# Optimization experiments

Hardware: AMD Instinct MI355X
Metric: run time of the kernel (lower is better)

The kernel has to match this reference:

```python
import jax, jax.numpy as jnp
import numpy as np
import math

B, L, D, K = 4, 2048, 1024, 3
PAD = K // 2
EPS_LN = 1e-5
EPS_NORM = 1e-12


def dwsep_conv(x_bld, dw, dwb, pw, pwb):
    # x_bld: [B, L, D] -> depthwise conv over L (groups=D) then pointwise 1x1
    x = jnp.transpose(x_bld, (0, 2, 1))  # [B, D, L]
    y = jax.lax.conv_general_dilated(
        x, dw, window_strides=(1,), padding=[(PAD, PAD)],
        feature_group_count=D, dimension_numbers=("NCH", "OIH", "NCH"))
    y = y + dwb[None, :, None]
    y = jnp.einsum("bcl,oc->bol", y, pw) + pwb[None, :, None]
    return jnp.transpose(y, (0, 2, 1))  # [B, L, D]


def l2norm(x):
    n = jnp.sqrt(jnp.sum(x * x, axis=-1, keepdims=True))
    return x / jnp.maximum(n, EPS_NORM)


def layernorm(x, g, b):
    mu = jnp.mean(x, axis=-1, keepdims=True)
    var = jnp.mean((x - mu) ** 2, axis=-1, keepdims=True)
    return (x - mu) * jax.lax.rsqrt(var + EPS_LN) * g + b


def setup_inputs() -> dict:
    key = jax.random.key(0)
    ks = jax.random.split(key, 24)
    s = 0.02
    def w(k, shape, scale=s):
        return (jax.random.normal(k, shape, dtype=jnp.float32) * scale)
    inp = {
        "x": jax.random.normal(ks[0], (B, L, D), dtype=jnp.float32),
        "wq": w(ks[1], (D, D)), "bq": jnp.zeros((D,), jnp.float32),
        "wk": w(ks[2], (D, D)), "bk": jnp.zeros((D,), jnp.float32),
        "wv": w(ks[3], (D, D)), "bv": jnp.zeros((D,), jnp.float32),
        "dwq": w(ks[4], (D, 1, K), 0.1), "dwq_b": jnp.zeros((D,), jnp.float32),
        "pwq": w(ks[5], (D, D)), "pwq_b": jnp.zeros((D,), jnp.float32),
        "dwk": w(ks[6], (D, 1, K), 0.1), "dwk_b": jnp.zeros((D,), jnp.float32),
        "pwk": w(ks[7], (D, D)), "pwk_b": jnp.zeros((D,), jnp.float32),
        "dwv": w(ks[8], (D, 1, K), 0.1), "dwv_b": jnp.zeros((D,), jnp.float32),
        "pwv": w(ks[9], (D, D)), "pwv_b": jnp.zeros((D,), jnp.float32),
        "wg": w(ks[10], (D, D)), "bg": jnp.zeros((D,), jnp.float32),
        "wo": w(ks[11], (D, D)), "bo": jnp.zeros((D,), jnp.float32),
        "mem_w": w(ks[12], (D, D)),
        "ln_g": jnp.ones((D,), jnp.float32),
        "ln_b": jnp.zeros((D,), jnp.float32),
    }
    return inp


def reference(x, wq, bq, wk, bk, wv, bv,
              dwq, dwq_b, pwq, pwq_b,
              dwk, dwk_b, pwk, pwk_b,
              dwv, dwv_b, pwv, pwv_b,
              wg, bg, wo, bo, mem_w, ln_g, ln_b):
    residual = x
    Q = jax.nn.silu(jnp.einsum("bld,ed->ble", x, wq) + bq)
    Kt = jax.nn.silu(jnp.einsum("bld,ed->ble", x, wk) + bk)
    V = jax.nn.silu(jnp.einsum("bld,ed->ble", x, wv) + bv)
    Q = dwsep_conv(Q, dwq, dwq_b, pwq, pwq_b)
    Kt = dwsep_conv(Kt, dwk, dwk_b, pwk, pwk_b)
    V = dwsep_conv(V, dwv, dwv_b, pwv, pwv_b)
    Qn = l2norm(Q)
    Kn = l2norm(Kt)
    scores = jnp.einsum("bqd,bkd->bqk", Qn, Kn) / math.sqrt(D)
    attn = jax.nn.softmax(scores, axis=-1)
    attn_out = jnp.einsum("bqk,bkd->bqd", attn, V)
    gate = jax.nn.sigmoid(jnp.einsum("bld,ed->ble", attn_out, wg) + bg)
    gated = gate * attn_out
    out = jnp.einsum("bld,ed->ble", gated, wo) + bo + residual
    out = layernorm(out, ln_g, ln_b)
    mem_pred = jnp.einsum("bld,de->ble", Kn, mem_w)
    mem_loss = jnp.mean((mem_pred - V) ** 2)
    return (out, mem_loss)
```

## Files before the change

kernel.cpp:

```cpp
#include <hip/hip_runtime.h>
#include <stdint.h>

typedef __attribute__((ext_vector_type(8))) short short8;
typedef __attribute__((ext_vector_type(4))) short short4v;
typedef __attribute__((ext_vector_type(4))) float f32x4;

#define DEV static __device__ __forceinline__

static constexpr int LL = 2048;
static constexpr int DD = 1024;
static constexpr long long BLD = 8388608LL;
static constexpr long long SLD = 2097152LL;
static constexpr long long SLLB = 4194304LL;

DEV short f2bf(float f) {
    uint32_t u = __builtin_bit_cast(uint32_t, f);
    u += 0x7fffu + ((u >> 16) & 1u);
    return (short)(u >> 16);
}
DEV float bf2f(short s) {
    uint32_t u = ((uint32_t)(uint16_t)s) << 16;
    return __builtin_bit_cast(float, u);
}

DEV float waveSum(float v) {
#pragma unroll
    for (int o = 32; o; o >>= 1) v += __shfl_down(v, o);
    return v;
}

DEV void gload16(const void* g, void* l) {
    __builtin_amdgcn_global_load_lds(
        (const __attribute__((address_space(1))) uint32_t*)(uintptr_t)g,
        (__attribute__((address_space(3))) uint32_t*)(uintptr_t)l,
        16, 0, 0);
}

__global__ __launch_bounds__(256) void k_prep(
    const float* __restrict__ x,
    const float* wq, const float* wk, const float* wv,
    const float* pq, const float* pk, const float* pv,
    const float* wg, const float* wo,
    const float* bq, const float* bk, const float* bv,
    const float* pqb, const float* pkb, const float* pvb,
    const float* __restrict__ memw,
    short* Wqkv, short* Pqkv, short* Wg, short* Wo,
    float* bqkv, float* bpw, short* MwT, short* xb, float* loss,
    float* rsum) {
    __shared__ float tile[64][65];
    const int bid = blockIdx.x;
    const int t = threadIdx.x;

    if (bid < 4096) {
        const int w = bid >> 9;
        const long long i = (long long)((bid & 511) * 256 + t) * 8;
        const float* src; short* dst;
        switch (w) {
            case 0: src = wq; dst = Wqkv;                break;
            case 1: src = wk; dst = Wqkv + 1048576;      break;
            case 2: src = wv; dst = Wqkv + 2097152;      break;
            case 3: src = pq; dst = Pqkv;                break;
            case 4: src = pk; dst = Pqkv + 1048576;      break;
            case 5: src = pv; dst = Pqkv + 2097152;      break;
            case 6: src = wg; dst = Wg;                  break;
            default: src = wo; dst = Wo;                 break;
        }
        const float4* p = (const float4*)(src + i);
        float4 a = p[0], b = p[1];
        short8 o;
        o[0] = f2bf(a.x); o[1] = f2bf(a.y); o[2] = f2bf(a.z); o[3] = f2bf(a.w);
        o[4] = f2bf(b.x); o[5] = f2bf(b.y); o[6] = f2bf(b.z); o[7] = f2bf(b.w);
        *(short8*)(dst + i) = o;
    } else if (bid < 4120) {
        const int idx = (bid - 4096) * 256 + t;
        const int sel = idx >> 10, j = idx & 1023;
        const float* s;
        switch (sel) {
            case 0: s = bq; break; case 1: s = bk; break; case 2: s = bv; break;
            case 3: s = pqb; break; case 4: s = pkb; break; default: s = pvb; break;
        }
        float v = s[j];
        if (sel < 3) bqkv[sel * 1024 + j] = v;
        else         bpw[(sel - 3) * 1024 + j] = v;
    } else if (bid < 4376) {
        const int tt = bid - 4120;
        const int r0 = (tt >> 4) * 64, c0 = (tt & 15) * 64;
#pragma unroll
        for (int i = 0; i < 16; i++) {
            int lin = i * 256 + t; int lr = lin >> 6, lc = lin & 63;
            tile[lr][lc] = memw[(long long)(r0 + lr) * DD + (c0 + lc)];
        }
        __syncthreads();
#pragma unroll
        for (int i = 0; i < 16; i++) {
            int lin = i * 256 + t; int orr = lin >> 6, oc = lin & 63;
            MwT[(long long)(c0 + orr) * DD + (r0 + oc)] = f2bf(tile[oc][orr]);
        }
    } else if (bid < 8472) {
        const long long i = (long long)((bid - 4376) * 256 + t) * 8;
        const float4* p = (const float4*)(x + i);
        float4 a = p[0], b = p[1];
        short8 o;
        o[0] = f2bf(a.x); o[1] = f2bf(a.y); o[2] = f2bf(a.z); o[3] = f2bf(a.w);
        o[4] = f2bf(b.x); o[5] = f2bf(b.y); o[6] = f2bf(b.z); o[7] = f2bf(b.w);
        *(short8*)(xb + i) = o;
    } else if (bid == 8472) {
        if (t == 0) *loss = 0.f;
    } else {
        rsum[(bid - 8473) * 256 + t] = 0.f;
    }
}

__global__ __launch_bounds__(256) void k_dwconv3b(const short* __restrict__ in,
                                                  const float* __restrict__ dwq,
                                                  const float* __restrict__ dwk,
                                                  const float* __restrict__ dwv,
                                                  const float* __restrict__ dbq,
                                                  const float* __restrict__ dbk,
                                                  const float* __restrict__ dbv,
                                                  short* __restrict__ outp) {
    const int idx = blockIdx.x * 256 + threadIdx.x;
    const int d8 = idx & 127;
    const int lc = (idx >> 7) & 255;
    const int b  = (idx >> 15) & 3;
    const int br = idx >> 17;
    const float* dw = (br == 0) ? dwq : (br == 1) ? dwk : dwv;
    const float* db = (br == 0) ? dbq : (br == 1) ? dbk : dbv;

    float w[24], bb[8];
    {
        const float4* wp = (const float4*)(dw + d8 * 24);
#pragma unroll
        for (int i = 0; i < 6; i++) {
            float4 tt = wp[i];
            w[i * 4 + 0] = tt.x; w[i * 4 + 1] = tt.y;
            w[i * 4 + 2] = tt.z; w[i * 4 + 3] = tt.w;
        }
        const float4* bp = (const float4*)(db + d8 * 8);
        float4 t0 = bp[0], t1 = bp[1];
        bb[0] = t0.x; bb[1] = t0.y; bb[2] = t0.z; bb[3] = t0.w;
        bb[4] = t1.x; bb[5] = t1.y; bb[6] = t1.z; bb[7] = t1.w;
    }

    const int l0 = lc * 8;
    const long long base = ((long long)(b * LL + l0)) * 3072 + br * 1024 + d8 * 8;
    short8 xr[10];
#pragma unroll
    for (int i = 0; i < 10; i++) {
        const int l = l0 - 1 + i;
        if (l >= 0 && l < LL) xr[i] = *(const short8*)(in + base + (long long)(i - 1) * 3072);
        else { short8 z = {0, 0, 0, 0, 0, 0, 0, 0}; xr[i] = z; }
    }
#pragma unroll
    for (int j = 0; j < 8; j++) {
        short8 o;
#pragma unroll
        for (int c = 0; c < 8; c++) {
            float v = bb[c] + w[c * 3 + 0] * bf2f(xr[j][c])
                            + w[c * 3 + 1] * bf2f(xr[j + 1][c])
                            + w[c * 3 + 2] * bf2f(xr[j + 2][c]);
            o[c] = f2bf(v);
        }
        *(short8*)(outp + base + (long long)j * 3072) = o;
    }
}

__global__ __launch_bounds__(256) void k_vt_norm(const short* __restrict__ vb,
                                                 short* __restrict__ VT,
                                                 const short* __restrict__ qkb,
                                                 float* __restrict__ ninv) {
    __shared__ short tile[64][65];
    __shared__ float red[4];
    const int bid = blockIdx.x;
    const int t = threadIdx.x;
    if (bid < 2048) {
        const int z = bid >> 9, tt = bid & 511;
        const int r0 = (tt >> 4) * 64, c0 = (tt & 15) * 64;
        const short* in = vb + (long long)z * SLD;
        short* out = VT + (long long)z * SLD;
#pragma unroll
        for (int i = 0; i < 16; i++) {
            int lin = i * 256 + t; int lr = lin >> 6, lc = lin & 63;
            tile[lr][lc] = in[(long long)(r0 + lr) * 1024 + (c0 + lc)];
        }
        __syncthreads();
#pragma unroll
        for (int i = 0; i < 16; i++) {
            int lin = i * 256 + t; int orr = lin >> 6, oc = lin & 63;
            out[(long long)(c0 + orr) * 2048 + (r0 + oc)] = tile[oc][orr];
        }
    } else {
        const long long row = bid - 2048;
        const short* p = qkb + row * DD;
        short4v v = *(const short4v*)(p + t * 4);
        float f0 = bf2f(v[0]), f1 = bf2f(v[1]), f2 = bf2f(v[2]), f3 = bf2f(v[3]);
        float ss = f0 * f0 + f1 * f1 + f2 * f2 + f3 * f3;
        ss = waveSum(ss);
        if ((t & 63) == 0) red[t >> 6] = ss;
        __syncthreads();
        ss = (red[0] + red[1]) + (red[2] + red[3]);
        if (t == 0) ninv[row] = 1.f / fmaxf(sqrtf(ss), 1e-12f);
    }
}

__global__ __launch_bounds__(256) void k_layernorm(float* __restrict__ y,
                                                   const float* __restrict__ g,
                                                   const float* __restrict__ b) {
    __shared__ float redS[4], redQ[4];
    const long long row = blockIdx.x;
    float* p = y + row * DD;
    const int t = threadIdx.x;
    float4 v = *(float4*)(p + t * 4);
    float s = v.x + v.y + v.z + v.w;
    float q = v.x * v.x + v.y * v.y + v.z * v.z + v.w * v.w;
    s = waveSum(s); q = waveSum(q);
    if ((t & 63) == 0) { redS[t >> 6] = s; redQ[t >> 6] = q; }
    __syncthreads();
    s = (redS[0] + redS[1]) + (redS[2] + redS[3]);
    q = (redQ[0] + redQ[1]) + (redQ[2] + redQ[3]);
    float mu = s * (1.f / DD);
    float var = q * (1.f / DD) - mu * mu;
    float rs = rsqrtf(var + 1e-5f);
    float4 o;
    o.x = (v.x - mu) * rs * g[t * 4 + 0] + b[t * 4 + 0];
    o.y = (v.y - mu) * rs * g[t * 4 + 1] + b[t * 4 + 1];
    o.z = (v.z - mu) * rs * g[t * 4 + 2] + b[t * 4 + 2];
    o.w = (v.w - mu) * rs * g[t * 4 + 3] + b[t * 4 + 3];
    *(float4*)(p + t * 4) = o;
}

enum { EPI_SILU, EPI_BIAS, EPI_EXPS, EPI_GATE, EPI_RESID };

template <int EPI>
__global__ __launch_bounds__(256, 4) void gemm(
    const short* __restrict__ A, int lda, long long sAb,
    const short* __restrict__ W, int ldw, long long sWb,
    void* __restrict__ outv, int ldo, long long sOb,
    const float* __restrict__ bias, long long sBias,
    const void* __restrict__ aux,
    int K, float scale, float* __restrict__ rsum) {
    __shared__ short lds[16384];

    const int z = blockIdx.z;
    A += (long long)z * sAb;
    W += (long long)z * sWb;

    const int tid = threadIdx.x;
    const int wid = tid >> 6, lane = tid & 63;
    const int row0 = blockIdx.y * 128, col0 = blockIdx.x * 128;
    const int wrM = (wid >> 1) * 64, wcN = (wid & 1) * 64;
    const int rl = lane & 15, kcl = lane >> 4;

    f32x4 acc[4][4] = {};

    const int srow = tid >> 3;
    const int cswz = (tid & 7) ^ (srow & 7);
    long long offA[4], offB[4];
#pragma unroll
    for (int j = 0; j < 4; j++) {
        const int rr = j * 32 + srow;
        offA[j] = (long long)(row0 + rr) * lda + cswz * 8;
        offB[j] = (long long)(col0 + rr) * ldw + cswz * 8;
    }

    const int nk = K >> 6;
    const int swz0 = (kcl ^ (rl & 7)) * 8;
    const int swz1 = ((kcl + 4) ^ (rl & 7)) * 8;

    for (int t = 0; t < nk; ++t) {
        const short* a = A + (long long)t * 64;
        const short* w = W + (long long)t * 64;
#pragma unroll
        for (int j = 0; j < 4; j++)
            gload16(a + offA[j], lds + (j * 256 + tid) * 8);
#pragma unroll
        for (int j = 0; j < 4; j++)
            gload16(w + offB[j], lds + 8192 + (j * 256 + tid) * 8);
        asm volatile("s_waitcnt vmcnt(0)" ::: "memory");
        __builtin_amdgcn_s_barrier();

        short8 af[4], bfr[4];
#pragma unroll
        for (int mi = 0; mi < 4; mi++)
            af[mi] = *(const short8*)&lds[(wrM + mi * 16 + rl) * 64 + swz0];
#pragma unroll
        for (int ni = 0; ni < 4; ni++)
            bfr[ni] = *(const short8*)&lds[8192 + (wcN + ni * 16 + rl) * 64 + swz0];
        __builtin_amdgcn_s_setprio(1);
#pragma unroll
        for (int mi = 0; mi < 4; mi++)
#pragma unroll
            for (int ni = 0; ni < 4; ni++)
                acc[mi][ni] = __builtin_amdgcn_mfma_f32_16x16x32_bf16(
                    af[mi], bfr[ni], acc[mi][ni], 0, 0, 0);
        __builtin_amdgcn_s_setprio(0);
#pragma unroll
        for (int mi = 0; mi < 4; mi++)
            af[mi] = *(const short8*)&lds[(wrM + mi * 16 + rl) * 64 + swz1];
#pragma unroll
        for (int ni = 0; ni < 4; ni++)
            bfr[ni] = *(const short8*)&lds[8192 + (wcN + ni * 16 + rl) * 64 + swz1];
        __builtin_amdgcn_s_setprio(1);
#pragma unroll
        for (int mi = 0; mi < 4; mi++)
#pragma unroll
            for (int ni = 0; ni < 4; ni++)
                acc[mi][ni] = __builtin_amdgcn_mfma_f32_16x16x32_bf16(
                    af[mi], bfr[ni], acc[mi][ni], 0, 0, 0);
        __builtin_amdgcn_s_setprio(0);
        __builtin_amdgcn_s_barrier();
    }

    const int lr4 = (lane >> 4) * 4;
    if constexpr (EPI == EPI_EXPS) {
        const float* qz = bias + (long long)z * sBias;
        const float* kz = (const float*)aux + (long long)z * 2048;
        float* rs = rsum + (long long)z * 2048;
        short* op = (short*)outv + (long long)z * sOb;
        float kc4[4];
#pragma unroll
        for (int ni = 0; ni < 4; ni++) kc4[ni] = kz[col0 + wcN + ni * 16 + rl];
#pragma unroll
        for (int mi = 0; mi < 4; mi++) {
            float ps[4] = {0.f, 0.f, 0.f, 0.f};
#pragma unroll
            for (int ni = 0; ni < 4; ni++) {
                const int gc = col0 + wcN + ni * 16 + rl;
#pragma unroll
                for (int r = 0; r < 4; r++) {
                    const int gr = row0 + wrM + mi * 16 + lr4 + r;
                    float p = __expf(acc[mi][ni][r] * qz[gr] * kc4[ni] * scale);
                    op[(long long)gr * ldo + gc] = f2bf(p);
                    ps[r] += p;
                }
            }
#pragma unroll
            for (int r = 0; r < 4; r++) {
                float v = ps[r];
                v += __shfl_xor(v, 1);
                v += __shfl_xor(v, 2);
                v += __shfl_xor(v, 4);
                v += __shfl_xor(v, 8);
                if ((lane & 15) == 0)
                    atomicAdd(&rs[row0 + wrM + mi * 16 + lr4 + r], v);
            }
        }
    } else {
        float bcol[4];
        const float* bz = bias + (long long)z * sBias;
#pragma unroll
        for (int ni = 0; ni < 4; ni++) bcol[ni] = bz[col0 + wcN + ni * 16 + rl];
#pragma unroll
        for (int mi = 0; mi < 4; mi++) {
#pragma unroll
            for (int ni = 0; ni < 4; ni++) {
                const int gc = col0 + wcN + ni * 16 + rl;
#pragma unroll
                for (int r = 0; r < 4; r++) {
                    const int gr = row0 + wrM + mi * 16 + lr4 + r;
                    const long long oi = (long long)gr * ldo + gc;
                    float v = acc[mi][ni][r];
                    if constexpr (EPI == EPI_SILU) {
                        v += bcol[ni];
                        v = v / (1.f + __expf(-v));
                        ((short*)outv + (long long)z * sOb)[oi] = f2bf(v);
                    } else if constexpr (EPI == EPI_BIAS) {
                        ((short*)outv + (long long)z * sOb)[oi] = f2bf(v + bcol[ni]);
                    } else if constexpr (EPI == EPI_GATE) {
                        float g = 1.f / (1.f + __expf(-(v + bcol[ni])));
                        float a = bf2f(((const short*)aux)[oi]);
                        ((short*)outv)[oi] = f2bf(g * a);
                    } else if constexpr (EPI == EPI_RESID) {
                        ((float*)outv)[oi] = v + bcol[ni] + ((const float*)aux)[oi];
                    }
                }
            }
        }
    }
}

__global__ __launch_bounds__(256, 4) void k_avml(
    const short* __restrict__ P, const short* __restrict__ VT,
    const float* __restrict__ rsum, short* __restrict__ aob,
    const short* __restrict__ kb, const short* __restrict__ MwT,
    const short* __restrict__ vb, const float* __restrict__ kinv,
    float* __restrict__ lossOut) {
    __shared__ short lds[16384];

    const int bid = blockIdx.x;
    const int xcd = bid & 7, j = bid >> 3;
    const bool isAV = j < 64;
    const short* A; const short* W;
    int lda, ldw, K, row0, col0;
    const float* rp = nullptr;
    short* outp = nullptr;
    if (isAV) {
        const int strip = xcd * 8 + (j >> 3);
        const int z = strip >> 4;
        row0 = (strip & 15) * 128; col0 = (j & 7) * 128;
        A = P + (long long)z * SLLB;  lda = 2048;
        W = VT + (long long)z * SLD;  ldw = 2048;
        K = 2048;
        outp = aob + (long long)z * SLD;
        rp = rsum + z * 2048;
    } else {
        const int jj = j - 64;
        const int strip = xcd * 8 + (jj >> 3);
        row0 = strip * 128; col0 = (jj & 7) * 128;
        A = kb; lda = 1024; W = MwT; ldw = 1024; K = 1024;
    }

    const int tid = threadIdx.x;
    const int wid = tid >> 6, lane = tid & 63;
    const int wrM = (wid >> 1) * 64, wcN = (wid & 1) * 64;
    const int rl = lane & 15, kcl = lane >> 4;

    f32x4 acc[4][4] = {};

    const int srow = tid >> 3;
    const int cswz = (tid & 7) ^ (srow & 7);
    long long offA[4], offB[4];
#pragma unroll
    for (int jj = 0; jj < 4; jj++) {
        const int rr = jj * 32 + srow;
        offA[jj] = (long long)(row0 + rr) * lda + cswz * 8;
        offB[jj] = (long long)(col0 + rr) * ldw + cswz * 8;
    }

    const int nk = K >> 6;
    const int swz0 = (kcl ^ (rl & 7)) * 8;
    const int swz1 = ((kcl + 4) ^ (rl & 7)) * 8;

    for (int t = 0; t < nk; ++t) {
        const short* a = A + (long long)t * 64;
        const short* w = W + (long long)t * 64;
#pragma unroll
        for (int jj = 0; jj < 4; jj++)
            gload16(a + offA[jj], lds + (jj * 256 + tid) * 8);
#pragma unroll
        for (int jj = 0; jj < 4; jj++)
            gload16(w + offB[jj], lds + 8192 + (jj * 256 + tid) * 8);
        asm volatile("s_waitcnt vmcnt(0)" ::: "memory");
        __builtin_amdgcn_s_barrier();

        short8 af[4], bfr[4];
#pragma unroll
        for (int mi = 0; mi < 4; mi++)
            af[mi] = *(const short8*)&lds[(wrM + mi * 16 + rl) * 64 + swz0];
#pragma unroll
        for (int ni = 0; ni < 4; ni++)
            bfr[ni] = *(const short8*)&lds[8192 + (wcN + ni * 16 + rl) * 64 + swz0];
        __builtin_amdgcn_s_setprio(1);
#pragma unroll
        for (int mi = 0; mi < 4; mi++)
#pragma unroll
            for (int ni = 0; ni < 4; ni++)
                acc[mi][ni] = __builtin_amdgcn_mfma_f32_16x16x32_bf16(
                    af[mi], bfr[ni], acc[mi][ni], 0, 0, 0);
        __builtin_amdgcn_s_setprio(0);
#pragma unroll
        for (int mi = 0; mi < 4; mi++)
            af[mi] = *(const short8*)&lds[(wrM + mi * 16 + rl) * 64 + swz1];
#pragma unroll
        for (int ni = 0; ni < 4; ni++)
            bfr[ni] = *(const short8*)&lds[8192 + (wcN + ni * 16 + rl) * 64 + swz1];
        __builtin_amdgcn_s_setprio(1);
#pragma unroll
        for (int mi = 0; mi < 4; mi++)
#pragma unroll
            for (int ni = 0; ni < 4; ni++)
                acc[mi][ni] = __builtin_amdgcn_mfma_f32_16x16x32_bf16(
                    af[mi], bfr[ni], acc[mi][ni], 0, 0, 0);
        __builtin_amdgcn_s_setprio(0);
        __builtin_amdgcn_s_barrier();
    }

    const int lr4 = (lane >> 4) * 4;
    if (isAV) {
#pragma unroll
        for (int mi = 0; mi < 4; mi++) {
#pragma unroll
            for (int ni = 0; ni < 4; ni++) {
                const int gc = col0 + wcN + ni * 16 + rl;
#pragma unroll
                for (int r = 0; r < 4; r++) {
                    const int gr = row0 + wrM + mi * 16 + lr4 + r;
                    outp[(long long)gr * 1024 + gc] = f2bf(acc[mi][ni][r] / rp[gr]);
                }
            }
        }
    } else {
        float lsum = 0.f;
#pragma unroll
        for (int mi = 0; mi < 4; mi++) {
#pragma unroll
            for (int ni = 0; ni < 4; ni++) {
                const int gc = col0 + wcN + ni * 16 + rl;
#pragma unroll
                for (int r = 0; r < 4; r++) {
                    const int gr = row0 + wrM + mi * 16 + lr4 + r;
                    float dd = acc[mi][ni][r] * kinv[gr] - bf2f(vb[(long long)gr * 1024 + gc]);
                    lsum += dd * dd;
                }
            }
        }
        lsum = waveSum(lsum);
        if (lane == 0) atomicAdd(lossOut, lsum * (1.f / (float)BLD));
    }
}


extern "C" void kernel_launch(void* const* d_in, const int* in_sizes, int n_in,
                              void* d_out, int out_size, void* d_ws, size_t ws_size,
                              hipStream_t stream) {
    const float* x    = (const float*)d_in[0];
    const float* wq   = (const float*)d_in[1];
    const float* bq   = (const float*)d_in[2];
    const float* wk   = (const float*)d_in[3];
    const float* bk   = (const float*)d_in[4];
    const float* wvw  = (const float*)d_in[5];
    const float* bvv  = (const float*)d_in[6];
    const float* dwq  = (const float*)d_in[7];
    const float* dwqb = (const float*)d_in[8];
    const float* pwq  = (const float*)d_in[9];
    const float* pwqb = (const float*)d_in[10];
    const float* dwk  = (const float*)d_in[11];
    const float* dwkb = (const float*)d_in[12];
    const float* pwk  = (const float*)d_in[13];
    const float* pwkb = (const float*)d_in[14];
    const float* dwv  = (const float*)d_in[15];
    const float* dwvb = (const float*)d_in[16];
    const float* pwv  = (const float*)d_in[17];
    const float* pwvb = (const float*)d_in[18];
    const float* wg   = (const float*)d_in[19];
    const float* bg   = (const float*)d_in[20];
    const float* wo   = (const float*)d_in[21];
    const float* bo   = (const float*)d_in[22];
    const float* memw = (const float*)d_in[23];
    const float* lng  = (const float*)d_in[24];
    const float* lnb  = (const float*)d_in[25];

    float* out = (float*)d_out;
    float* loss = out + BLD;

    char* base = (char*)d_ws;
    size_t off = 0;
    auto take = [&](size_t n) -> char* {
        char* p = base + off;
        off += (n + 255) & ~(size_t)255;
        return p;
    };
    const size_t WB = (size_t)DD * DD * 2;
    const size_t XB = (size_t)BLD * 2;
    short* Wqkv = (short*)take(3 * WB);
    short* Pqkv = (short*)take(3 * WB);
    short* Wgb  = (short*)take(WB);
    short* Wob  = (short*)take(WB);
    short* MwT  = (short*)take(WB);
    float* bqkv = (float*)take(3072 * 4);
    float* bpw  = (float*)take(3072 * 4);
    float* rsum = (float*)take(8192 * 4);
    float* ninv = (float*)take(16384 * 4);
    short* xb   = (short*)take(XB);
    short* pre  = (short*)take(3 * XB);
    short* post = (short*)take(3 * XB);

    short* qb = pre;
    short* kb = pre + BLD;
    short* vb = pre + 2 * BLD;
    short* scores = post;
    short* VT = post + 2 * BLD;
    short* aob = xb;
    short* gated = post;
    float* qinv = ninv;
    float* kinv = ninv + 8192;
    (void)ws_size; (void)in_sizes; (void)n_in; (void)out_size;

    const long long sLD = SLD;
    const long long sLLb = SLLB;

    k_prep<<<8505, 256, 0, stream>>>(
        x, wq, wk, wvw, pwq, pwk, pwv, wg, wo,
        bq, bk, bvv, pwqb, pwkb, pwvb, memw,
        Wqkv, Pqkv, Wgb, Wob, bqkv, bpw, MwT, xb, loss, rsum);

    gemm<EPI_SILU><<<dim3(24, 64, 1), 256, 0, stream>>>(
        xb, 1024, 0, Wqkv, 1024, 0, pre, 3072, 0, bqkv, 0, nullptr, 1024, 0.f, nullptr);

    k_dwconv3b<<<1536, 256, 0, stream>>>(pre, dwq, dwk, dwv, dwqb, dwkb, dwvb, post);

    gemm<EPI_BIAS><<<dim3(8, 64, 3), 256, 0, stream>>>(
        post, 3072, 1024, Pqkv, 1024, (long long)DD * DD, qb, 1024, BLD,
        bpw, 1024, nullptr, 1024, 0.f, nullptr);

    k_vt_norm<<<18432, 256, 0, stream>>>(vb, VT, qb, ninv);

    gemm<EPI_EXPS><<<dim3(16, 16, 4), 256, 0, stream>>>(
        qb, 1024, sLD, kb, 1024, sLD, scores, 2048, sLLb,
        qinv, 2048, kinv, 1024, 0.03125f, rsum);

    k_avml<<<1024, 256, 0, stream>>>(scores, VT, rsum, aob, kb, MwT, vb, kinv, loss);

    gemm<EPI_GATE><<<dim3(8, 64, 1), 256, 0, stream>>>(
        aob, 1024, 0, Wgb, 1024, 0, gated, 1024, 0, bg, 0, aob, 1024, 0.f, nullptr);

    gemm<EPI_RESID><<<dim3(8, 64, 1), 256, 0, stream>>>(
        gated, 1024, 0, Wob, 1024, 0, out, 1024, 0, bo, 0, x, 1024, 0.f, nullptr);
    k_layernorm<<<8192, 256, 0, stream>>>(out, lng, lnb);
}
```

Before: 345.0 us.

## Fuse Q/K sum-of-squares into pointwise GEMM epilogue and add XCD-aware block remap

The row sum-of-squares for Q and K is now accumulated with atomics inside the pointwise-conv GEMM epilogue, from the bf16-rounded outputs. This removes the separate norm pass that re-read Q and K; the inverse norm is computed on the fly in the score GEMM and loss epilogues. k_prep zeroes the new accumulator buffer. Several GEMMs also gain an XCD-aware block index remap so that blocks sharing row panels land on the same chiplet's L2. The cost is extra atomics, shuffles and per-use sqrt/divide work in the epilogues.

```diff
diff --git a/kernel.cpp b/kernel.cpp
--- a/kernel.cpp
+++ b/kernel.cpp
@@ -46,7 +46,7 @@
     const float* __restrict__ memw,
     short* Wqkv, short* Pqkv, short* Wg, short* Wo,
     float* bqkv, float* bpw, short* MwT, short* xb, float* loss,
-    float* rsum) {
+    float* rsum, float* ssq) {
     __shared__ float tile[64][65];
     const int bid = blockIdx.x;
     const int t = threadIdx.x;
@@ -106,8 +106,10 @@
         *(short8*)(xb + i) = o;
     } else if (bid == 8472) {
         if (t == 0) *loss = 0.f;
+    } else if (bid < 8505) {
+        rsum[(bid - 8473) * 256 + t] = 0.f;
     } else {
-        rsum[(bid - 8473) * 256 + t] = 0.f;
+        ssq[(bid - 8505) * 256 + t] = 0.f;
     }
 }
 
@@ -165,41 +167,25 @@
     }
 }
 
-__global__ __launch_bounds__(256) void k_vt_norm(const short* __restrict__ vb,
-                                                 short* __restrict__ VT,
-                                                 const short* __restrict__ qkb,
-                                                 float* __restrict__ ninv) {
+__global__ __launch_bounds__(256) void k_vt(const short* __restrict__ vb,
+                                            short* __restrict__ VT) {
     __shared__ short tile[64][65];
-    __shared__ float red[4];
     const int bid = blockIdx.x;
     const int t = threadIdx.x;
-    if (bid < 2048) {
-        const int z = bid >> 9, tt = bid & 511;
-        const int r0 = (tt >> 4) * 64, c0 = (tt & 15) * 64;
-        const short* in = vb + (long long)z * SLD;
-        short* out = VT + (long long)z * SLD;
-#pragma unroll
-        for (int i = 0; i < 16; i++) {
-            int lin = i * 256 + t; int lr = lin >> 6, lc = lin & 63;
-            tile[lr][lc] = in[(long long)(r0 + lr) * 1024 + (c0 + lc)];
-        }
-        __syncthreads();
-#pragma unroll
-        for (int i = 0; i < 16; i++) {
-            int lin = i * 256 + t; int orr = lin >> 6, oc = lin & 63;
-            out[(long long)(c0 + orr) * 2048 + (r0 + oc)] = tile[oc][orr];
-        }
-    } else {
-        const long long row = bid - 2048;
-        const short* p = qkb + row * DD;
-        short4v v = *(const short4v*)(p + t * 4);
-        float f0 = bf2f(v[0]), f1 = bf2f(v[1]), f2 = bf2f(v[2]), f3 = bf2f(v[3]);
-        float ss = f0 * f0 + f1 * f1 + f2 * f2 + f3 * f3;
-        ss = waveSum(ss);
-        if ((t & 63) == 0) red[t >> 6] = ss;
-        __syncthreads();
-        ss = (red[0] + red[1]) + (red[2] + red[3]);
-        if (t == 0) ninv[row] = 1.f / fmaxf(sqrtf(ss), 1e-12f);
+    const int z = bid >> 9, tt = bid & 511;
+    const int r0 = (tt >> 4) * 64, c0 = (tt & 15) * 64;
+    const short* in = vb + (long long)z * SLD;
+    short* out = VT + (long long)z * SLD;
+#pragma unroll
+    for (int i = 0; i < 16; i++) {
+        int lin = i * 256 + t; int lr = lin >> 6, lc = lin & 63;
+        tile[lr][lc] = in[(long long)(r0 + lr) * 1024 + (c0 + lc)];
+    }
+    __syncthreads();
+#pragma unroll
+    for (int i = 0; i < 16; i++) {
+        int lin = i * 256 + t; int orr = lin >> 6, oc = lin & 63;
+        out[(long long)(c0 + orr) * 2048 + (r0 + oc)] = tile[oc][orr];
     }
 }
 
@@ -229,9 +215,9 @@
     *(float4*)(p + t * 4) = o;
 }
 
-enum { EPI_SILU, EPI_BIAS, EPI_EXPS, EPI_GATE, EPI_RESID };
-
-template <int EPI>
+enum { EPI_SILU, EPI_PWQK, EPI_EXPS, EPI_GATE, EPI_RESID };
+
+template <int EPI, bool XCD>
 __global__ __launch_bounds__(256, 4) void gemm(
     const short* __restrict__ A, int lda, long long sAb,
     const short* __restrict__ W, int ldw, long long sWb,
@@ -241,13 +227,24 @@
     int K, float scale, float* __restrict__ rsum) {
     __shared__ short lds[16384];
 
-    const int z = blockIdx.z;
+    int bx = blockIdx.x, by = blockIdx.y, bz = blockIdx.z;
+    if constexpr (XCD) {
+        const int gx = gridDim.x, gy = gridDim.y;
+        const int nb = gx * gy * gridDim.z;
+        const int bid = bx + gx * (by + gy * bz);
+        const int xcd = bid & 7, r = bid >> 3;
+        const int spx = nb / (8 * gx);
+        const int sl = r / gx, cb = r - sl * gx;
+        const int sg = xcd * spx + sl;
+        bx = cb; by = sg % gy; bz = sg / gy;
+    }
+    const int z = bz;
     A += (long long)z * sAb;
     W += (long long)z * sWb;
 
     const int tid = threadIdx.x;
     const int wid = tid >> 6, lane = tid & 63;
-    const int row0 = blockIdx.y * 128, col0 = blockIdx.x * 128;
+    const int row0 = by * 128, col0 = bx * 128;
     const int wrM = (wid >> 1) * 64, wcN = (wid & 1) * 64;
     const int rl = lane & 15, kcl = lane >> 4;
 
@@ -319,17 +316,21 @@
         short* op = (short*)outv + (long long)z * sOb;
         float kc4[4];
 #pragma unroll
-        for (int ni = 0; ni < 4; ni++) kc4[ni] = kz[col0 + wcN + ni * 16 + rl];
+        for (int ni = 0; ni < 4; ni++) {
+            float ss = kz[col0 + wcN + ni * 16 + rl];
+            kc4[ni] = 1.f / fmaxf(sqrtf(ss), 1e-12f);
+        }
 #pragma unroll
         for (int mi = 0; mi < 4; mi++) {
             float ps[4] = {0.f, 0.f, 0.f, 0.f};
 #pragma unroll
-            for (int ni = 0; ni < 4; ni++) {
-                const int gc = col0 + wcN + ni * 16 + rl;
-#pragma unroll
-                for (int r = 0; r < 4; r++) {
-                    const int gr = row0 + wrM + mi * 16 + lr4 + r;
-                    float p = __expf(acc[mi][ni][r] * qz[gr] * kc4[ni] * scale);
+            for (int r = 0; r < 4; r++) {
+                const int gr = row0 + wrM + mi * 16 + lr4 + r;
+                float qv = 1.f / fmaxf(sqrtf(qz[gr]), 1e-12f);
+#pragma unroll
+                for (int ni = 0; ni < 4; ni++) {
+                    const int gc = col0 + wcN + ni * 16 + rl;
+                    float p = __expf(acc[mi][ni][r] * qv * kc4[ni] * scale);
                     op[(long long)gr * ldo + gc] = f2bf(p);
                     ps[r] += p;
                 }
@@ -352,6 +353,7 @@
         for (int ni = 0; ni < 4; ni++) bcol[ni] = bz[col0 + wcN + ni * 16 + rl];
 #pragma unroll
         for (int mi = 0; mi < 4; mi++) {
+            float ps[4] = {0.f, 0.f, 0.f, 0.f};
 #pragma unroll
             for (int ni = 0; ni < 4; ni++) {
                 const int gc = col0 + wcN + ni * 16 + rl;
@@ -364,8 +366,11 @@
                         v += bcol[ni];
                         v = v / (1.f + __expf(-v));
                         ((short*)outv + (long long)z * sOb)[oi] = f2bf(v);
-                    } else if constexpr (EPI == EPI_BIAS) {
-                        ((short*)outv + (long long)z * sOb)[oi] = f2bf(v + bcol[ni]);
+                    } else if constexpr (EPI == EPI_PWQK) {
+                        short h = f2bf(v + bcol[ni]);
+                        ((short*)outv + (long long)z * sOb)[oi] = h;
+                        float vr = bf2f(h);
+                        ps[r] += vr * vr;
                     } else if constexpr (EPI == EPI_GATE) {
                         float g = 1.f / (1.f + __expf(-(v + bcol[ni])));
                         float a = bf2f(((const short*)aux)[oi]);
@@ -375,6 +380,21 @@
                     }
                 }
             }
+            if constexpr (EPI == EPI_PWQK) {
+                if (z < 2) {
+                    float* sq = rsum + (long long)z * 8192;
+#pragma unroll
+                    for (int r = 0; r < 4; r++) {
+                        float v = ps[r];
+                        v += __shfl_xor(v, 1);
+                        v += __shfl_xor(v, 2);
+                        v += __shfl_xor(v, 4);
+                        v += __shfl_xor(v, 8);
+                        if ((lane & 15) == 0)
+                            atomicAdd(&sq[row0 + wrM + mi * 16 + lr4 + r], v);
+                    }
+                }
+            }
         }
     }
 }
@@ -383,7 +403,7 @@
     const short* __restrict__ P, const short* __restrict__ VT,
     const float* __restrict__ rsum, short* __restrict__ aob,
     const short* __restrict__ kb, const short* __restrict__ MwT,
-    const short* __restrict__ vb, const float* __restrict__ kinv,
+    const short* __restrict__ vb, const float* __restrict__ ssk,
     float* __restrict__ lossOut) {
     __shared__ short lds[16384];
 
@@ -494,12 +514,13 @@
 #pragma unroll
         for (int mi = 0; mi < 4; mi++) {
 #pragma unroll
-            for (int ni = 0; ni < 4; ni++) {
-                const int gc = col0 + wcN + ni * 16 + rl;
-#pragma unroll
-                for (int r = 0; r < 4; r++) {
-                    const int gr = row0 + wrM + mi * 16 + lr4 + r;
-                    float dd = acc[mi][ni][r] * kinv[gr] - bf2f(vb[(long long)gr * 1024 + gc]);
+            for (int r = 0; r < 4; r++) {
+                const int gr = row0 + wrM + mi * 16 + lr4 + r;
+                const float kiv = 1.f / fmaxf(sqrtf(ssk[gr]), 1e-12f);
+#pragma unroll
+                for (int ni = 0; ni < 4; ni++) {
+                    const int gc = col0 + wcN + ni * 16 + rl;
+                    float dd = acc[mi][ni][r] * kiv - bf2f(vb[(long long)gr * 1024 + gc]);
                     lsum += dd * dd;
                 }
             }
@@ -560,7 +581,7 @@
     float* bqkv = (float*)take(3072 * 4);
     float* bpw  = (float*)take(3072 * 4);
     float* rsum = (float*)take(8192 * 4);
-    float* ninv = (float*)take(16384 * 4);
+    float* ssq  = (float*)take(16384 * 4);
     short* xb   = (short*)take(XB);
     short* pre  = (short*)take(3 * XB);
     short* post = (short*)take(3 * XB);
@@ -572,39 +593,38 @@
     short* VT = post + 2 * BLD;
     short* aob = xb;
     short* gated = post;
-    float* qinv = ninv;
-    float* kinv = ninv + 8192;
+    float* ssq_k = ssq + 8192;
     (void)ws_size; (void)in_sizes; (void)n_in; (void)out_size;
 
     const long long sLD = SLD;
     const long long sLLb = SLLB;
 
-    k_prep<<<8505, 256, 0, stream>>>(
+    k_prep<<<8569, 256, 0, stream>>>(
         x, wq, wk, wvw, pwq, pwk, pwv, wg, wo,
         bq, bk, bvv, pwqb, pwkb, pwvb, memw,
-        Wqkv, Pqkv, Wgb, Wob, bqkv, bpw, MwT, xb, loss, rsum);
-
-    gemm<EPI_SILU><<<dim3(24, 64, 1), 256, 0, stream>>>(
+        Wqkv, Pqkv, Wgb, Wob, bqkv, bpw, MwT, xb, loss, rsum, ssq);
+
+    gemm<EPI_SILU, true><<<dim3(24, 64, 1), 256, 0, stream>>>(
         xb, 1024, 0, Wqkv, 1024, 0, pre, 3072, 0, bqkv, 0, nullptr, 1024, 0.f, nullptr);
 
     k_dwconv3b<<<1536, 256, 0, stream>>>(pre, dwq, dwk, dwv, dwqb, dwkb, dwvb, post);
 
-    gemm<EPI_BIAS><<<dim3(8, 64, 3), 256, 0, stream>>>(
+    gemm<EPI_PWQK, true><<<dim3(8, 64, 3), 256, 0, stream>>>(
         post, 3072, 1024, Pqkv, 1024, (long long)DD * DD, qb, 1024, BLD,
-        bpw, 1024, nullptr, 1024, 0.f, nullptr);
-
-    k_vt_norm<<<18432, 256, 0, stream>>>(vb, VT, qb, ninv);
-
-    gemm<EPI_EXPS><<<dim3(16, 16, 4), 256, 0, stream>>>(
+        bpw, 1024, nullptr, 1024, 0.f, ssq);
+
+    k_vt<<<2048, 256, 0, stream>>>(vb, VT);
+
+    gemm<EPI_EXPS, true><<<dim3(16, 16, 4), 256, 0, stream>>>(
         qb, 1024, sLD, kb, 1024, sLD, scores, 2048, sLLb,
-        qinv, 2048, kinv, 1024, 0.03125f, rsum);
-
-    k_avml<<<1024, 256, 0, stream>>>(scores, VT, rsum, aob, kb, MwT, vb, kinv, loss);
-
-    gemm<EPI_GATE><<<dim3(8, 64, 1), 256, 0, stream>>>(
+        ssq, 2048, ssq_k, 1024, 0.03125f, rsum);
+
+    k_avml<<<1024, 256, 0, stream>>>(scores, VT, rsum, aob, kb, MwT, vb, ssq_k, loss);
+
+    gemm<EPI_GATE, false><<<dim3(8, 64, 1), 256, 0, stream>>>(
         aob, 1024, 0, Wgb, 1024, 0, gated, 1024, 0, bg, 0, aob, 1024, 0.f, nullptr);
 
-    gemm<EPI_RESID><<<dim3(8, 64, 1), 256, 0, stream>>>(
+    gemm<EPI_RESID, false><<<dim3(8, 64, 1), 256, 0, stream>>>(
         gated, 1024, 0, Wob, 1024, 0, out, 1024, 0, bo, 0, x, 1024, 0.f, nullptr);
     k_layernorm<<<8192, 256, 0, stream>>>(out, lng, lnb);
 }
```

Result: no change. 338.7 us (-1.8%).
